# Kernel optimization log

Measured on AMD Instinct MI355X. Metric: run time of the kernel, lower is better.

## Reference

```python
import jax, jax.numpy as jnp
import numpy as np
from jax.ops import segment_sum

NUM_GRAPHS = 64


def _leaky_relu(x):
    return jnp.where(x >= 0, x, 0.01 * x)


def setup_inputs() -> dict:
    key = jax.random.key(0)
    ks = jax.random.split(key, 8)
    N, E, D = 100000, 1600000, 128
    x = jax.random.normal(ks[0], (N, D), dtype=jnp.float32)
    edge_index = jax.random.randint(ks[1], (2, E), 0, N, dtype=jnp.int64)
    batch = jnp.sort(jax.random.randint(ks[2], (N,), 0, NUM_GRAPHS, dtype=jnp.int64))
    s = 1.0 / np.sqrt(D)
    W1 = jax.random.normal(ks[3], (D, D), dtype=jnp.float32) * s
    b1 = jnp.zeros((D,), dtype=jnp.float32)
    W2 = jax.random.normal(ks[4], (D, D), dtype=jnp.float32) * s
    b2 = jnp.zeros((D,), dtype=jnp.float32)
    fcW = jax.random.normal(ks[5], (D, 1), dtype=jnp.float32) * s
    fcb = jnp.zeros((1,), dtype=jnp.float32)
    return {"x": x, "edge_index": edge_index, "batch": batch,
            "W1": W1, "b1": b1, "W2": W2, "b2": b2, "fcW": fcW, "fcb": fcb}


def reference(x, edge_index, batch, W1, b1, W2, b2, fcW, fcb):
    N = x.shape[0]
    # GCNConv: add self-loops, symmetric normalization D^-1/2 A D^-1/2
    loop = jnp.arange(N, dtype=edge_index.dtype)
    row = jnp.concatenate([edge_index[0], loop])  # source j
    col = jnp.concatenate([edge_index[1], loop])  # target i
    deg = segment_sum(jnp.ones_like(col, dtype=x.dtype), col, num_segments=N)
    dis = jax.lax.rsqrt(deg)  # deg >= 1 due to self-loops
    norm = dis[row] * dis[col]  # [E+N]

    def conv(h, W, b):
        h = h @ W                               # [N, D'] linear transform
        msg = h[row] * norm[:, None]            # gather + scale
        agg = segment_sum(msg, col, num_segments=N)  # scatter-add
        return agg + b

    h = _leaky_relu(conv(x, W1, b1))
    h = _leaky_relu(conv(h, W2, b2))

    # global_mean_pool over batch ids
    sums = segment_sum(h, batch, num_segments=NUM_GRAPHS)
    cnts = segment_sum(jnp.ones((N,), dtype=h.dtype), batch, num_segments=NUM_GRAPHS)
    pooled = sums / jnp.maximum(cnts, 1.0)[:, None]
    return pooled @ fcW + fcb  # [NUM_GRAPHS, 1]
```

## Files before the change

### kernel.cpp

```cpp
#include <hip/hip_runtime.h>
#include <hip/hip_bf16.h>
#include <math.h>

#define D 128
#define NUM_GRAPHS 64
#define CHUNK 8192
#define BUCK_SH 8
#define BUCK_N 256
#define BCAP 8192
#define PSLICE 8

typedef __bf16 bf16x8 __attribute__((ext_vector_type(8)));
typedef __bf16 bf16x2 __attribute__((ext_vector_type(2)));
typedef float f32x4 __attribute__((ext_vector_type(4)));
typedef float f32x2 __attribute__((ext_vector_type(2)));

__device__ inline unsigned char f32_to_fp8(float x) {
    int pk = __builtin_amdgcn_cvt_pk_fp8_f32(x, x, 0, false);
    return (unsigned char)(pk & 0xff);
}
__device__ inline f32x2 fp8x2_to_f32(unsigned short us) {
    return __builtin_amdgcn_cvt_pk_f32_fp8((unsigned int)us, false);
}

__global__ void k_prepW(const float* __restrict__ Wa, const float* __restrict__ Wb,
                        __bf16* __restrict__ WfA, __bf16* __restrict__ WfB,
                        float* __restrict__ pooled, int* __restrict__ done,
                        int* __restrict__ gcur,
                        const int* __restrict__ batch, int* __restrict__ gstart, int N) {
    int gid = blockIdx.x * 256 + threadIdx.x;
    if (gid < NUM_GRAPHS * D) pooled[gid] = 0.f;
    if (gid == 0) *done = 0;
    if (gid < 512) gcur[gid] = 0;
    if (gid >= 16384 && gid <= 16384 + NUM_GRAPHS) {
        int g = gid - 16384;
        int lo = 0, hi = N;
        while (lo < hi) { int mid = (lo + hi) >> 1; if (batch[mid] < g) lo = mid + 1; else hi = mid; }
        gstart[g] = lo;
    }
    if (gid >= 32768) return;
    const float* W = (gid < 16384) ? Wa : Wb;
    __bf16* Wf = (gid < 16384) ? WfA : WfB;
    int idx = gid & 16383;
    int j = idx & 7, lane = (idx >> 3) & 63, kc = (idx >> 9) & 3, ft = idx >> 11;
    int k = kc * 32 + (lane >> 4) * 8 + j;
    int f = ft * 16 + (lane & 15);
    Wf[idx] = (__bf16)W[k * D + f];
}

__global__ void k_bin(const int* __restrict__ ei, int* __restrict__ gcur,
                      int* __restrict__ bbuf, int nbuck, int E) {
    __shared__ int h[512];
    __shared__ int base[512];
    int tid = threadIdx.x;
    for (int b = tid; b < nbuck; b += 256) h[b] = 0;
    __syncthreads();
    int lo = blockIdx.x * CHUNK;
    if (lo + CHUNK <= E) {
        const int4* c4 = (const int4*)(ei + E + lo);
#pragma unroll 2
        for (int i = tid; i < CHUNK / 4; i += 256) {
            int4 c = c4[i];
            atomicAdd(&h[c.x >> BUCK_SH], 1);
            atomicAdd(&h[c.y >> BUCK_SH], 1);
            atomicAdd(&h[c.z >> BUCK_SH], 1);
            atomicAdd(&h[c.w >> BUCK_SH], 1);
        }
    } else {
        for (int i = tid; i < CHUNK; i += 256) {
            int e = lo + i;
            if (e < E) atomicAdd(&h[ei[E + e] >> BUCK_SH], 1);
        }
    }
    __syncthreads();
    for (int b = tid; b < nbuck; b += 256) {
        base[b] = atomicAdd(&gcur[b], h[b]);
        h[b] = 0;
    }
    __syncthreads();
    if (lo + CHUNK <= E) {
        const int4* r4 = (const int4*)(ei + lo);
        const int4* c4 = (const int4*)(ei + E + lo);
#pragma unroll 2
        for (int i = tid; i < CHUNK / 4; i += 256) {
            int4 r = r4[i];
            int4 c = c4[i];
            int rr[4] = {r.x, r.y, r.z, r.w};
            int cc[4] = {c.x, c.y, c.z, c.w};
#pragma unroll
            for (int u = 0; u < 4; u++) {
                int b = cc[u] >> BUCK_SH;
                int pos = base[b] + atomicAdd(&h[b], 1);
                if (pos < BCAP) bbuf[(size_t)b * BCAP + pos] = rr[u] | ((cc[u] & (BUCK_N - 1)) << 17);
            }
        }
    } else {
        for (int i = tid; i < CHUNK; i += 256) {
            int e = lo + i;
            if (e < E) {
                int r = ei[e], c = ei[E + e];
                int b = c >> BUCK_SH;
                int pos = base[b] + atomicAdd(&h[b], 1);
                if (pos < BCAP) bbuf[(size_t)b * BCAP + pos] = r | ((c & (BUCK_N - 1)) << 17);
            }
        }
    }
}

__global__ void k_place(const int* __restrict__ bbuf, const int* __restrict__ gcur,
                        int* __restrict__ esrc,
                        int* __restrict__ cnt, int* __restrict__ offs,
                        float* __restrict__ dis, int N) {
    __shared__ int h[256];
    __shared__ int sc[256];
    __shared__ int cur[256];
    int b = blockIdx.x, tid = threadIdx.x;
    int start = b * BCAP;
    int count = gcur[b]; if (count > BCAP) count = BCAP;
    int end = start + count;
    h[tid] = 0;
    __syncthreads();
    for (int i = start + tid; i < end; i += 256) atomicAdd(&h[(bbuf[i] >> 17) & 255], 1);
    __syncthreads();
    int local = h[tid];
    sc[tid] = local;
    __syncthreads();
    for (int off = 1; off < 256; off <<= 1) {
        int xv = (tid >= off) ? sc[tid - off] : 0;
        __syncthreads();
        sc[tid] += xv;
        __syncthreads();
    }
    int excl = sc[tid] - local;
    cur[tid] = start + excl;
    int c = b * 256 + tid;
    if (c < N) {
        cnt[c]  = local;
        offs[c] = start + excl;
        dis[c]  = rsqrtf(1.0f + (float)local);
    }
    __syncthreads();
    for (int i = start + tid; i < end; i += 256) {
        int p = bbuf[i];
        int pos = atomicAdd(&cur[(p >> 17) & 255], 1);
        esrc[pos] = p & 0x1FFFF;
    }
}

template <typename T>
__launch_bounds__(256)
__global__ void k_gemm(const T* __restrict__ X, const __bf16* __restrict__ Wfrag,
                       const float* __restrict__ dis, unsigned char* __restrict__ Y8, int N) {
    int tid = threadIdx.x;
    int w = tid >> 6, lane = tid & 63;
    int quad = lane >> 4, m = lane & 15;
    int nodeA = blockIdx.x * 64 + w * 16 + m;
    if (nodeA >= N) nodeA = N - 1;

    bf16x8 a[4];
#pragma unroll
    for (int kc = 0; kc < 4; kc++) {
        int kb = kc * 32 + quad * 8;
        if constexpr (sizeof(T) == 4) {
            f32x4 x0 = *(const f32x4*)(X + (size_t)nodeA * D + kb);
            f32x4 x1 = *(const f32x4*)(X + (size_t)nodeA * D + kb + 4);
#pragma unroll
            for (int j = 0; j < 4; j++) { a[kc][j] = (__bf16)x0[j]; a[kc][4 + j] = (__bf16)x1[j]; }
        } else {
            a[kc] = *(const bf16x8*)(X + (size_t)nodeA * D + kb);
        }
    }

    f32x4 d[8];
#pragma unroll
    for (int ft = 0; ft < 8; ft++) {
        d[ft] = (f32x4){0.f, 0.f, 0.f, 0.f};
#pragma unroll
        for (int kc = 0; kc < 4; kc++) {
            bf16x8 b = *(const bf16x8*)(Wfrag + (((ft << 2) | kc) * 64 + lane) * 8);
            d[ft] = __builtin_amdgcn_mfma_f32_16x16x32_bf16(a[kc], b, d[ft], 0, 0, 0);
        }
    }

#pragma unroll
    for (int r = 0; r < 4; r++) {
        int node = blockIdx.x * 64 + w * 16 + quad * 4 + r;
        if (node < N) {
            float dv = dis[node];
#pragma unroll
            for (int ft = 0; ft < 8; ft++)
                Y8[(size_t)node * D + ft * 16 + m] = f32_to_fp8(d[ft][r] * dv);
        }
    }
}

__launch_bounds__(256)
__global__ void k_agg(const unsigned char* __restrict__ Hs8, __bf16* __restrict__ O,
                      const int* __restrict__ offs, const int* __restrict__ cnt,
                      const float* __restrict__ dis, const int* __restrict__ esrc,
                      const float* __restrict__ bias, int N) {
    int wave = (blockIdx.x * 256 + threadIdx.x) >> 6;
    int lane = threadIdx.x & 63;
    int node0 = wave * 8;
    float b0 = bias[lane * 2], b1 = bias[lane * 2 + 1];

    for (int nn = 0; nn < 8; nn++) {
        int node = node0 + nn;
        if (node >= N) return;
        int start = offs[node];
        int len = cnt[node];
        float di = dis[node];
        f32x2 h = fp8x2_to_f32(*(const unsigned short*)(Hs8 + (size_t)node * D + lane * 2));
        float acc0 = h[0];
        float acc1 = h[1];

        for (int k0 = 0; k0 < len; k0 += 64) {
            int mm = len - k0; if (mm > 64) mm = 64;
            int ep = esrc[start + k0 + (lane < mm ? lane : 0)];
            int j = 0;
            for (; j + 16 <= mm; j += 16) {
                int s[16]; unsigned short hv[16];
#pragma unroll
                for (int u = 0; u < 16; u++) s[u] = __shfl(ep, j + u);
#pragma unroll
                for (int u = 0; u < 16; u++) hv[u] = *(const unsigned short*)(Hs8 + (size_t)s[u] * D + lane * 2);
#pragma unroll
                for (int u = 0; u < 16; u++) { f32x2 f = fp8x2_to_f32(hv[u]); acc0 += f[0]; acc1 += f[1]; }
            }
            for (; j + 4 <= mm; j += 4) {
                int s[4]; unsigned short hv[4];
#pragma unroll
                for (int u = 0; u < 4; u++) s[u] = __shfl(ep, j + u);
#pragma unroll
                for (int u = 0; u < 4; u++) hv[u] = *(const unsigned short*)(Hs8 + (size_t)s[u] * D + lane * 2);
#pragma unroll
                for (int u = 0; u < 4; u++) { f32x2 f = fp8x2_to_f32(hv[u]); acc0 += f[0]; acc1 += f[1]; }
            }
            for (; j < mm; j++) {
                int s = __shfl(ep, j);
                f32x2 f = fp8x2_to_f32(*(const unsigned short*)(Hs8 + (size_t)s * D + lane * 2));
                acc0 += f[0]; acc1 += f[1];
            }
        }

        acc0 = acc0 * di + b0;
        acc1 = acc1 * di + b1;
        acc0 = acc0 >= 0.f ? acc0 : 0.01f * acc0;
        acc1 = acc1 >= 0.f ? acc1 : 0.01f * acc1;
        bf16x2 o; o[0] = (__bf16)acc0; o[1] = (__bf16)acc1;
        *(bf16x2*)(O + (size_t)node * D + lane * 2) = o;
    }
}

__launch_bounds__(256)
__global__ void k_pool(const __bf16* __restrict__ H, const int* __restrict__ gstart,
                       float* __restrict__ pooled,
                       const float* __restrict__ fcW, const float* __restrict__ fcb,
                       float* __restrict__ out, int* __restrict__ done) {
    __shared__ float sdata[256 * 9];
    __shared__ int lastflag;
    int g = blockIdx.x / PSLICE;
    int slice = blockIdx.x - g * PSLICE;
    int gs = gstart[g], ge = gstart[g + 1];
    int cg = ge - gs;
    int r0 = gs + (int)((long long)cg * slice / PSLICE);
    int r1 = gs + (int)((long long)cg * (slice + 1) / PSLICE);
    int t = threadIdx.x;
    int rg = t >> 4, fb = t & 15;

    float acc[8];
#pragma unroll
    for (int j = 0; j < 8; j++) acc[j] = 0.f;
    for (int r = r0 + rg; r < r1; r += 16) {
        bf16x8 v = *(const bf16x8*)(H + (size_t)r * D + fb * 8);
#pragma unroll
        for (int j = 0; j < 8; j++) acc[j] += (float)v[j];
    }
#pragma unroll
    for (int j = 0; j < 8; j++) sdata[t * 9 + j] = acc[j];
    __syncthreads();
#pragma unroll
    for (int s = 128; s >= 16; s >>= 1) {
        if (t < s) {
#pragma unroll
            for (int j = 0; j < 8; j++) sdata[t * 9 + j] += sdata[(t + s) * 9 + j];
        }
        __syncthreads();
    }
    if (t < 16) {
#pragma unroll
        for (int j = 0; j < 8; j++) atomicAdd(&pooled[g * D + t * 8 + j], sdata[t * 9 + j]);
    }
    __threadfence();
    __syncthreads();
    if (t == 0) lastflag = (atomicAdd(done, 1) == (int)gridDim.x - 1) ? 1 : 0;
    __syncthreads();
    if (lastflag) {
        __threadfence();
        if (t < NUM_GRAPHS) {
            float s = 0.f;
#pragma unroll 4
            for (int k = 0; k < D; k++) s += pooled[t * D + k] * fcW[k];
            float c = (float)(gstart[t + 1] - gstart[t]);
            out[t] = s / fmaxf(c, 1.0f) + fcb[0];
        }
    }
}

extern "C" void kernel_launch(void* const* d_in, const int* in_sizes, int n_in,
                              void* d_out, int out_size, void* d_ws, size_t ws_size,
                              hipStream_t stream) {
    const float* x    = (const float*)d_in[0];
    const int*   ei   = (const int*)d_in[1];
    const int*   batch= (const int*)d_in[2];
    const float* W1   = (const float*)d_in[3];
    const float* b1   = (const float*)d_in[4];
    const float* W2   = (const float*)d_in[5];
    const float* b2   = (const float*)d_in[6];
    const float* fcW  = (const float*)d_in[7];
    const float* fcb  = (const float*)d_in[8];
    float* out = (float*)d_out;

    int N = in_sizes[0] / D;
    int E = in_sizes[1] / 2;

    int NBUCK  = (N + BUCK_N - 1) >> BUCK_SH;
    int NCHUNK = (E + CHUNK - 1) / CHUNK;

    char* p = (char*)d_ws;
    auto alloc = [&](size_t bytes) { char* r = p; p += (bytes + 255) & ~(size_t)255; return r; };
    int*    cnt    = (int*)   alloc((size_t)N * 4);
    int*    offs   = (int*)   alloc((size_t)N * 4);
    float*  dis    = (float*) alloc((size_t)N * 4);
    int*    gcur   = (int*)   alloc(512 * 4);
    int*    bbuf   = (int*)   alloc((size_t)NBUCK * BCAP * 4);
    int*    esrc   = (int*)   alloc((size_t)NBUCK * BCAP * 4);
    unsigned char* bufA8 = (unsigned char*)alloc((size_t)N * D);
    __bf16* bufB   = (__bf16*)alloc((size_t)N * D * 2);
    __bf16* Wf1    = (__bf16*)alloc((size_t)D * D * 2);
    __bf16* Wf2    = (__bf16*)alloc((size_t)D * D * 2);
    float*  pooled = (float*) alloc((size_t)NUM_GRAPHS * D * 4);
    int*    gstart = (int*)   alloc((NUM_GRAPHS + 1) * 4);
    int*    done   = (int*)   alloc(256);

    k_prepW<<<129, 256, 0, stream>>>(W1, W2, Wf1, Wf2, pooled, done, gcur, batch, gstart, N);

    k_bin  <<<NCHUNK, 256, 0, stream>>>(ei, gcur, bbuf, NBUCK, E);
    k_place<<<NBUCK, 256, 0, stream>>>(bbuf, gcur, esrc, cnt, offs, dis, N);

    int gblocks = (N + 63) / 64;
    int ablocks = (N + 31) / 32;

    k_gemm<float><<<gblocks, 256, 0, stream>>>(x, Wf1, dis, bufA8, N);
    k_agg<<<ablocks, 256, 0, stream>>>(bufA8, bufB, offs, cnt, dis, esrc, b1, N);
    k_gemm<__bf16><<<gblocks, 256, 0, stream>>>(bufB, Wf2, dis, bufA8, N);
    k_agg<<<ablocks, 256, 0, stream>>>(bufA8, bufB, offs, cnt, dis, esrc, b2, N);
    k_pool<<<NUM_GRAPHS * PSLICE, 256, 0, stream>>>(bufB, gstart, pooled, fcW, fcb, out, done);
}
```

Baseline: 315.0 us.

## Overlap first GEMM with edge binning and fuse pooling into final aggregation

The first GEMM no longer needs per-node degree scaling, so it runs in the same launch as the edge-binning kernel and overlaps with it. The source-side normalization moves into aggregation as a per-edge dis multiply, broadcast by shuffle. The second aggregation accumulates mean-pool partial sums directly with atomics and runs the final FC in its last block, which removes the bf16 write and re-read and the separate pool kernel. In exchange the aggregation does extra dis gathers and multiplies per edge and issues more pooled atomics, and the fp8 values are now stored unscaled, which may change precision.

```diff
diff --git a/kernel.cpp b/kernel.cpp
--- a/kernel.cpp
+++ b/kernel.cpp
@@ -8,7 +8,6 @@
 #define BUCK_SH 8
 #define BUCK_N 256
 #define BCAP 8192
-#define PSLICE 8
 
 typedef __bf16 bf16x8 __attribute__((ext_vector_type(8)));
 typedef __bf16 bf16x2 __attribute__((ext_vector_type(2)));
@@ -48,10 +47,64 @@
     Wf[idx] = (__bf16)W[k * D + f];
 }
 
-__global__ void k_bin(const int* __restrict__ ei, int* __restrict__ gcur,
-                      int* __restrict__ bbuf, int nbuck, int E) {
+template <typename T>
+__device__ __forceinline__ void gemm_body(int bid, int tid, const T* __restrict__ X,
+                                          const __bf16* __restrict__ Wfrag,
+                                          unsigned char* __restrict__ Y8, int N) {
+    int w = tid >> 6, lane = tid & 63;
+    int quad = lane >> 4, m = lane & 15;
+    int nodeA = bid * 64 + w * 16 + m;
+    if (nodeA >= N) nodeA = N - 1;
+
+    bf16x8 a[4];
+#pragma unroll
+    for (int kc = 0; kc < 4; kc++) {
+        int kb = kc * 32 + quad * 8;
+        if constexpr (sizeof(T) == 4) {
+            f32x4 x0 = *(const f32x4*)(X + (size_t)nodeA * D + kb);
+            f32x4 x1 = *(const f32x4*)(X + (size_t)nodeA * D + kb + 4);
+#pragma unroll
+            for (int j = 0; j < 4; j++) { a[kc][j] = (__bf16)x0[j]; a[kc][4 + j] = (__bf16)x1[j]; }
+        } else {
+            a[kc] = *(const bf16x8*)(X + (size_t)nodeA * D + kb);
+        }
+    }
+
+    f32x4 d[8];
+#pragma unroll
+    for (int ft = 0; ft < 8; ft++) {
+        d[ft] = (f32x4){0.f, 0.f, 0.f, 0.f};
+#pragma unroll
+        for (int kc = 0; kc < 4; kc++) {
+            bf16x8 b = *(const bf16x8*)(Wfrag + (((ft << 2) | kc) * 64 + lane) * 8);
+            d[ft] = __builtin_amdgcn_mfma_f32_16x16x32_bf16(a[kc], b, d[ft], 0, 0, 0);
+        }
+    }
+
+#pragma unroll
+    for (int r = 0; r < 4; r++) {
+        int node = bid * 64 + w * 16 + quad * 4 + r;
+        if (node < N) {
+#pragma unroll
+            for (int ft = 0; ft < 8; ft++)
+                Y8[(size_t)node * D + ft * 16 + m] = f32_to_fp8(d[ft][r]);
+        }
+    }
+}
+
+__launch_bounds__(256)
+__global__ void k_bin_gemm(const int* __restrict__ ei, int* __restrict__ gcur,
+                           int* __restrict__ bbuf, int nbuck, int E, int nchunk,
+                           const float* __restrict__ X, const __bf16* __restrict__ Wfrag,
+                           unsigned char* __restrict__ Y8, int N) {
     __shared__ int h[512];
     __shared__ int base[512];
+
+    if (blockIdx.x >= nchunk) {
+        gemm_body<float>(blockIdx.x - nchunk, threadIdx.x, X, Wfrag, Y8, N);
+        return;
+    }
+
     int tid = threadIdx.x;
     for (int b = tid; b < nbuck; b += 256) h[b] = 0;
     __syncthreads();
@@ -147,99 +200,68 @@
     }
 }
 
-template <typename T>
 __launch_bounds__(256)
-__global__ void k_gemm(const T* __restrict__ X, const __bf16* __restrict__ Wfrag,
-                       const float* __restrict__ dis, unsigned char* __restrict__ Y8, int N) {
-    int tid = threadIdx.x;
-    int w = tid >> 6, lane = tid & 63;
-    int quad = lane >> 4, m = lane & 15;
-    int nodeA = blockIdx.x * 64 + w * 16 + m;
-    if (nodeA >= N) nodeA = N - 1;
-
-    bf16x8 a[4];
-#pragma unroll
-    for (int kc = 0; kc < 4; kc++) {
-        int kb = kc * 32 + quad * 8;
-        if constexpr (sizeof(T) == 4) {
-            f32x4 x0 = *(const f32x4*)(X + (size_t)nodeA * D + kb);
-            f32x4 x1 = *(const f32x4*)(X + (size_t)nodeA * D + kb + 4);
-#pragma unroll
-            for (int j = 0; j < 4; j++) { a[kc][j] = (__bf16)x0[j]; a[kc][4 + j] = (__bf16)x1[j]; }
-        } else {
-            a[kc] = *(const bf16x8*)(X + (size_t)nodeA * D + kb);
-        }
-    }
-
-    f32x4 d[8];
-#pragma unroll
-    for (int ft = 0; ft < 8; ft++) {
-        d[ft] = (f32x4){0.f, 0.f, 0.f, 0.f};
-#pragma unroll
-        for (int kc = 0; kc < 4; kc++) {
-            bf16x8 b = *(const bf16x8*)(Wfrag + (((ft << 2) | kc) * 64 + lane) * 8);
-            d[ft] = __builtin_amdgcn_mfma_f32_16x16x32_bf16(a[kc], b, d[ft], 0, 0, 0);
-        }
-    }
-
-#pragma unroll
-    for (int r = 0; r < 4; r++) {
-        int node = blockIdx.x * 64 + w * 16 + quad * 4 + r;
-        if (node < N) {
-            float dv = dis[node];
-#pragma unroll
-            for (int ft = 0; ft < 8; ft++)
-                Y8[(size_t)node * D + ft * 16 + m] = f32_to_fp8(d[ft][r] * dv);
-        }
-    }
-}
-
+__global__ void k_gemm2(const __bf16* __restrict__ X, const __bf16* __restrict__ Wfrag,
+                        unsigned char* __restrict__ Y8, int N) {
+    gemm_body<__bf16>(blockIdx.x, threadIdx.x, X, Wfrag, Y8, N);
+}
+
+template <int POOL>
 __launch_bounds__(256)
 __global__ void k_agg(const unsigned char* __restrict__ Hs8, __bf16* __restrict__ O,
                       const int* __restrict__ offs, const int* __restrict__ cnt,
                       const float* __restrict__ dis, const int* __restrict__ esrc,
-                      const float* __restrict__ bias, int N) {
+                      const float* __restrict__ bias,
+                      const int* __restrict__ batch, float* __restrict__ pooled,
+                      const float* __restrict__ fcW, const float* __restrict__ fcb,
+                      float* __restrict__ out, const int* __restrict__ gstart,
+                      int* __restrict__ done, int N) {
     int wave = (blockIdx.x * 256 + threadIdx.x) >> 6;
     int lane = threadIdx.x & 63;
     int node0 = wave * 8;
     float b0 = bias[lane * 2], b1 = bias[lane * 2 + 1];
 
+    float s0 = 0.f, s1 = 0.f;
+    int curg = -1;
+
     for (int nn = 0; nn < 8; nn++) {
         int node = node0 + nn;
-        if (node >= N) return;
+        if (node >= N) break;
         int start = offs[node];
         int len = cnt[node];
         float di = dis[node];
         f32x2 h = fp8x2_to_f32(*(const unsigned short*)(Hs8 + (size_t)node * D + lane * 2));
-        float acc0 = h[0];
-        float acc1 = h[1];
+        float acc0 = h[0] * di;
+        float acc1 = h[1] * di;
 
         for (int k0 = 0; k0 < len; k0 += 64) {
             int mm = len - k0; if (mm > 64) mm = 64;
             int ep = esrc[start + k0 + (lane < mm ? lane : 0)];
+            float dvl = dis[ep];
             int j = 0;
             for (; j + 16 <= mm; j += 16) {
-                int s[16]; unsigned short hv[16];
-#pragma unroll
-                for (int u = 0; u < 16; u++) s[u] = __shfl(ep, j + u);
+                int s[16]; float dv[16]; unsigned short hv[16];
+#pragma unroll
+                for (int u = 0; u < 16; u++) { s[u] = __shfl(ep, j + u); dv[u] = __shfl(dvl, j + u); }
 #pragma unroll
                 for (int u = 0; u < 16; u++) hv[u] = *(const unsigned short*)(Hs8 + (size_t)s[u] * D + lane * 2);
 #pragma unroll
-                for (int u = 0; u < 16; u++) { f32x2 f = fp8x2_to_f32(hv[u]); acc0 += f[0]; acc1 += f[1]; }
+                for (int u = 0; u < 16; u++) { f32x2 f = fp8x2_to_f32(hv[u]); acc0 += f[0] * dv[u]; acc1 += f[1] * dv[u]; }
             }
             for (; j + 4 <= mm; j += 4) {
-                int s[4]; unsigned short hv[4];
-#pragma unroll
-                for (int u = 0; u < 4; u++) s[u] = __shfl(ep, j + u);
+                int s[4]; float dv[4]; unsigned short hv[4];
+#pragma unroll
+                for (int u = 0; u < 4; u++) { s[u] = __shfl(ep, j + u); dv[u] = __shfl(dvl, j + u); }
 #pragma unroll
                 for (int u = 0; u < 4; u++) hv[u] = *(const unsigned short*)(Hs8 + (size_t)s[u] * D + lane * 2);
 #pragma unroll
-                for (int u = 0; u < 4; u++) { f32x2 f = fp8x2_to_f32(hv[u]); acc0 += f[0]; acc1 += f[1]; }
+                for (int u = 0; u < 4; u++) { f32x2 f = fp8x2_to_f32(hv[u]); acc0 += f[0] * dv[u]; acc1 += f[1] * dv[u]; }
             }
             for (; j < mm; j++) {
                 int s = __shfl(ep, j);
+                float dv = __shfl(dvl, j);
                 f32x2 f = fp8x2_to_f32(*(const unsigned short*)(Hs8 + (size_t)s * D + lane * 2));
-                acc0 += f[0]; acc1 += f[1];
+                acc0 += f[0] * dv; acc1 += f[1] * dv;
             }
         }
 
@@ -247,62 +269,43 @@
         acc1 = acc1 * di + b1;
         acc0 = acc0 >= 0.f ? acc0 : 0.01f * acc0;
         acc1 = acc1 >= 0.f ? acc1 : 0.01f * acc1;
-        bf16x2 o; o[0] = (__bf16)acc0; o[1] = (__bf16)acc1;
-        *(bf16x2*)(O + (size_t)node * D + lane * 2) = o;
-    }
-}
-
-__launch_bounds__(256)
-__global__ void k_pool(const __bf16* __restrict__ H, const int* __restrict__ gstart,
-                       float* __restrict__ pooled,
-                       const float* __restrict__ fcW, const float* __restrict__ fcb,
-                       float* __restrict__ out, int* __restrict__ done) {
-    __shared__ float sdata[256 * 9];
-    __shared__ int lastflag;
-    int g = blockIdx.x / PSLICE;
-    int slice = blockIdx.x - g * PSLICE;
-    int gs = gstart[g], ge = gstart[g + 1];
-    int cg = ge - gs;
-    int r0 = gs + (int)((long long)cg * slice / PSLICE);
-    int r1 = gs + (int)((long long)cg * (slice + 1) / PSLICE);
-    int t = threadIdx.x;
-    int rg = t >> 4, fb = t & 15;
-
-    float acc[8];
-#pragma unroll
-    for (int j = 0; j < 8; j++) acc[j] = 0.f;
-    for (int r = r0 + rg; r < r1; r += 16) {
-        bf16x8 v = *(const bf16x8*)(H + (size_t)r * D + fb * 8);
-#pragma unroll
-        for (int j = 0; j < 8; j++) acc[j] += (float)v[j];
-    }
-#pragma unroll
-    for (int j = 0; j < 8; j++) sdata[t * 9 + j] = acc[j];
-    __syncthreads();
-#pragma unroll
-    for (int s = 128; s >= 16; s >>= 1) {
-        if (t < s) {
-#pragma unroll
-            for (int j = 0; j < 8; j++) sdata[t * 9 + j] += sdata[(t + s) * 9 + j];
-        }
+
+        if constexpr (POOL) {
+            int g = batch[node];
+            if (g != curg) {
+                if (curg >= 0) {
+                    atomicAdd(&pooled[curg * D + lane * 2],     s0);
+                    atomicAdd(&pooled[curg * D + lane * 2 + 1], s1);
+                }
+                curg = g; s0 = 0.f; s1 = 0.f;
+            }
+            s0 += acc0; s1 += acc1;
+        } else {
+            bf16x2 o; o[0] = (__bf16)acc0; o[1] = (__bf16)acc1;
+            *(bf16x2*)(O + (size_t)node * D + lane * 2) = o;
+        }
+    }
+
+    if constexpr (POOL) {
+        if (curg >= 0) {
+            atomicAdd(&pooled[curg * D + lane * 2],     s0);
+            atomicAdd(&pooled[curg * D + lane * 2 + 1], s1);
+        }
+        __shared__ int lastflag;
+        __threadfence();
         __syncthreads();
-    }
-    if (t < 16) {
-#pragma unroll
-        for (int j = 0; j < 8; j++) atomicAdd(&pooled[g * D + t * 8 + j], sdata[t * 9 + j]);
-    }
-    __threadfence();
-    __syncthreads();
-    if (t == 0) lastflag = (atomicAdd(done, 1) == (int)gridDim.x - 1) ? 1 : 0;
-    __syncthreads();
-    if (lastflag) {
-        __threadfence();
-        if (t < NUM_GRAPHS) {
-            float s = 0.f;
+        if (threadIdx.x == 0) lastflag = (atomicAdd(done, 1) == (int)gridDim.x - 1) ? 1 : 0;
+        __syncthreads();
+        if (lastflag) {
+            __threadfence();
+            int t = threadIdx.x;
+            if (t < NUM_GRAPHS) {
+                float s = 0.f;
 #pragma unroll 4
-            for (int k = 0; k < D; k++) s += pooled[t * D + k] * fcW[k];
-            float c = (float)(gstart[t + 1] - gstart[t]);
-            out[t] = s / fmaxf(c, 1.0f) + fcb[0];
+                for (int k = 0; k < D; k++) s += pooled[t * D + k] * fcW[k];
+                float c = (float)(gstart[t + 1] - gstart[t]);
+                out[t] = s / fmaxf(c, 1.0f) + fcb[0];
+            }
         }
     }
 }
@@ -343,17 +346,18 @@
     int*    gstart = (int*)   alloc((NUM_GRAPHS + 1) * 4);
     int*    done   = (int*)   alloc(256);
 
-    k_prepW<<<129, 256, 0, stream>>>(W1, W2, Wf1, Wf2, pooled, done, gcur, batch, gstart, N);
-
-    k_bin  <<<NCHUNK, 256, 0, stream>>>(ei, gcur, bbuf, NBUCK, E);
-    k_place<<<NBUCK, 256, 0, stream>>>(bbuf, gcur, esrc, cnt, offs, dis, N);
-
     int gblocks = (N + 63) / 64;
     int ablocks = (N + 31) / 32;
 
-    k_gemm<float><<<gblocks, 256, 0, stream>>>(x, Wf1, dis, bufA8, N);
-    k_agg<<<ablocks, 256, 0, stream>>>(bufA8, bufB, offs, cnt, dis, esrc, b1, N);
-    k_gemm<__bf16><<<gblocks, 256, 0, stream>>>(bufB, Wf2, dis, bufA8, N);
-    k_agg<<<ablocks, 256, 0, stream>>>(bufA8, bufB, offs, cnt, dis, esrc, b2, N);
-    k_pool<<<NUM_GRAPHS * PSLICE, 256, 0, stream>>>(bufB, gstart, pooled, fcW, fcb, out, done);
-}
+    k_prepW<<<129, 256, 0, stream>>>(W1, W2, Wf1, Wf2, pooled, done, gcur, batch, gstart, N);
+
+    k_bin_gemm<<<NCHUNK + gblocks, 256, 0, stream>>>(ei, gcur, bbuf, NBUCK, E, NCHUNK,
+                                                     x, Wf1, bufA8, N);
+    k_place<<<NBUCK, 256, 0, stream>>>(bbuf, gcur, esrc, cnt, offs, dis, N);
+
+    k_agg<0><<<ablocks, 256, 0, stream>>>(bufA8, bufB, offs, cnt, dis, esrc, b1,
+                                          batch, pooled, fcW, fcb, out, gstart, done, N);
+    k_gemm2<<<gblocks, 256, 0, stream>>>(bufB, Wf2, bufA8, N);
+    k_agg<1><<<ablocks, 256, 0, stream>>>(bufA8, nullptr, offs, cnt, dis, esrc, b2,
+                                          batch, pooled, fcW, fcb, out, gstart, done, N);
+}
```

After: 595.1 us. 88.9% more time.
